# Optimization experiments

Measured on AMD Instinct MI355X. Metric: run time of the kernel, lower is better.

## Reference

```python
import jax, jax.numpy as jnp
import numpy as np

H = 8          # num_heads
T = 2          # num_edge_types
NEG_SLOPE = 0.2


def _edge_softmax(scores, dst, num_nodes):
    # softmax over incoming edges of each destination node, per head
    m = jax.ops.segment_max(scores, dst, num_segments=num_nodes)  # [N,H]
    e = jnp.exp(scores - m[dst])                                   # [E,H]
    s = jax.ops.segment_sum(e, dst, num_segments=num_nodes)        # [N,H]
    return e / s[dst]


def setup_inputs() -> dict:
    key = jax.random.key(0)
    ks = jax.random.split(key, 8)
    N, D, E = 50000, 128, 800000
    return {
        "x": jax.random.normal(ks[0], (N, D), dtype=jnp.float32),
        "w_u": jax.random.normal(ks[1], (H * T, D), dtype=jnp.float32) * (1.0 / np.sqrt(D)),
        "b_u": jax.random.normal(ks[2], (H * T,), dtype=jnp.float32) * 0.01,
        "w_v": jax.random.normal(ks[3], (H * T, D), dtype=jnp.float32) * (1.0 / np.sqrt(D)),
        "src_e0": jax.random.randint(ks[4], (E,), 0, N, dtype=jnp.int32),
        "dst_e0": jax.random.randint(ks[5], (E,), 0, N, dtype=jnp.int32),
        "src_e1": jax.random.randint(ks[6], (E,), 0, N, dtype=jnp.int32),
        "dst_e1": jax.random.randint(ks[7], (E,), 0, N, dtype=jnp.int32),
    }


def reference(x, w_u, b_u, w_v, src_e0, dst_e0, src_e1, dst_e1):
    N, D = x.shape
    head_dim = D // H
    scores_u = x @ w_u.T + b_u   # [N, H*T]
    scores_v = x @ w_v.T         # [N, H*T]
    xh = x.reshape(N, head_dim, H)  # matches torch reshape(-1, head_dim, num_heads)
    outs = [x]  # sep=True
    for t, (src, dst) in enumerate([(src_e0, dst_e0), (src_e1, dst_e1)]):
        u = scores_u[:, t * H:(t + 1) * H]
        v = scores_v[:, t * H:(t + 1) * H]
        s = u[src] + v[dst]                         # u_add_v -> [E,H]
        s = jnp.where(s >= 0, s, NEG_SLOPE * s)     # LeakyReLU(0.2)
        p = _edge_softmax(s, dst, N)                # [E,H]
        msg = xh[src] * p[:, None, :]               # u_mul_e -> [E,head_dim,H]
        agg = jax.ops.segment_sum(msg, dst, num_segments=N)  # [N,head_dim,H]
        outs.append(agg.reshape(N, D))
    return jnp.concatenate(outs, axis=-1)  # [N, D*(1+T)]
```

## Files before the change

kernel.cpp:

```cpp
#include <hip/hip_runtime.h>

#define NEG_SLOPE 0.2f
#define RSHIFT 5
#define RW     32
#define MAXNR  1600
#define CHUNKP 8192

__device__ __forceinline__ ushort f2bf(float f) {
    union { float f; unsigned u; } c; c.f = f;
    unsigned u = c.u;
    return (ushort)((u + 0x7fffu + ((u >> 16) & 1u)) >> 16);
}
__device__ __forceinline__ float bflo(unsigned u) { return __uint_as_float(u << 16); }
__device__ __forceinline__ float bfhi(unsigned u) { return __uint_as_float(u & 0xffff0000u); }

__global__ __launch_bounds__(256) void mega_kernel(
    const float* __restrict__ x, const float* __restrict__ wu,
    const float* __restrict__ bu, const float* __restrict__ wv,
    const int* __restrict__ s0, const int* __restrict__ d0,
    const int* __restrict__ s1, const int* __restrict__ d1,
    float* __restrict__ out, ushort* __restrict__ xbf,
    float* __restrict__ su, float* __restrict__ sv,
    int* __restrict__ gcur, unsigned* __restrict__ pairs,
    int N, int E, int nr, int cap, int scoreBlocks, int ppset)
{
    __shared__ __align__(16) float smemf[32 * 129 + 16 * 132];
    int* smi = (int*)smemf;
    float* wlds = smemf;
    float* xtile = smemf + 32 * 129;
    int tid = threadIdx.x;
    int bid = blockIdx.x;

    if (bid < 2 * ppset) {
        int pb = bid;
        int t = pb / ppset, c = pb % ppset;
        const int* ss = t ? s1 : s0;
        const int* dd = t ? d1 : d0;
        int beg = c * CHUNKP, end = min(E, beg + CHUNKP);
        int* lcnt = smi; int* gb = smi + MAXNR; int* lrun = smi + 2 * MAXNR;
        for (int i = tid; i < nr; i += 256) lcnt[i] = 0;
        __syncthreads();
        for (int e = beg + tid; e < end; e += 256)
            atomicAdd(&lcnt[dd[e] >> RSHIFT], 1);
        __syncthreads();
        for (int i = tid; i < nr; i += 256) {
            gb[i] = atomicAdd(&gcur[t * nr + i], lcnt[i]);
            lrun[i] = 0;
        }
        __syncthreads();
        unsigned* pt = pairs + (size_t)t * nr * cap;
        for (int e = beg + tid; e < end; e += 256) {
            int dst = dd[e], src = ss[e];
            int rr = dst >> RSHIFT;
            int pos = atomicAdd(&lrun[rr], 1);
            pt[(size_t)rr * cap + gb[rr] + pos] = ((unsigned)dst << 16) | (unsigned)src;
        }
        return;
    }
    int nb = bid - 2 * ppset;
    int base = nb * 16;
    for (int i = tid; i < 4096; i += 256) {
        int o = i >> 7, k = i & 127;
        wlds[o * 129 + k] = (o < 16) ? wu[i] : wv[i - 2048];
    }
    for (int i2 = tid; i2 < 512; i2 += 256) {
        int I = nb * 512 + i2;
        int nl = i2 >> 5, q = i2 & 31;
        int n = base + nl;
        float4 v = make_float4(0.f, 0.f, 0.f, 0.f);
        if (n < N) {
            v = ((const float4*)x)[I];
            ((float4*)out)[(size_t)n * 96 + q] = v;
            ushort4 b;
            b.x = f2bf(v.x); b.y = f2bf(v.y); b.z = f2bf(v.z); b.w = f2bf(v.w);
            *(ushort4*)(xbf + (size_t)I * 4) = b;
        }
        ((float4*)(xtile + nl * 132))[q] = v;
    }
    __syncthreads();
    int o = tid & 15;
    int nl = tid >> 4;
    int n = base + nl;
    if (n >= N) return;
    const float4* xr4 = (const float4*)(xtile + nl * 132);
    const float* wur = wlds + o * 129;
    const float* wvr = wlds + (16 + o) * 129;
    float au = 0.f, av = 0.f;
#pragma unroll
    for (int kk = 0; kk < 32; ++kk) {
        float4 xv = xr4[kk];
        int k = kk * 4;
        au = fmaf(xv.x, wur[k],     au);  av = fmaf(xv.x, wvr[k],     av);
        au = fmaf(xv.y, wur[k + 1], au);  av = fmaf(xv.y, wvr[k + 1], av);
        au = fmaf(xv.z, wur[k + 2], au);  av = fmaf(xv.z, wvr[k + 2], av);
        au = fmaf(xv.w, wur[k + 3], au);  av = fmaf(xv.w, wvr[k + 3], av);
    }
    su[n * 16 + o] = au + bu[o];
    sv[n * 16 + o] = av;
}

__global__ __launch_bounds__(256, 8) void buildagg_kernel(
    const ushort* __restrict__ xbf, const float* __restrict__ su,
    const float* __restrict__ sv, const int* __restrict__ gcur,
    const unsigned* __restrict__ pairs, float* __restrict__ out,
    int N, int E, int nr, int cap)
{
    __shared__ ushort srcs[768];
    __shared__ int offl[33];
    __shared__ int cursor[32];
    __shared__ __align__(16) float ev4[4][512];
    int r = blockIdx.x, t = blockIdx.y, tid = threadIdx.x;
    int m = gcur[t * nr + r];
    if (m > cap) m = cap;
    const unsigned* p = pairs + ((size_t)t * nr + r) * cap;

    if (tid < 32) cursor[tid] = 0;
    __syncthreads();
    for (int i = tid; i < m; i += 256)
        atomicAdd(&cursor[(p[i] >> 16) & (RW - 1)], 1);
    __syncthreads();
    if (tid < 32) {
        int v = cursor[tid];
        int incl = v;
#pragma unroll
        for (int d = 1; d < 32; d <<= 1) {
            int o = __shfl(incl, tid - d);
            if (tid >= d) incl += o;
        }
        offl[tid + 1] = incl;
        if (tid == 0) offl[0] = 0;
        cursor[tid] = incl - v;
    }
    __syncthreads();
    for (int i = tid; i < m; i += 256) {
        unsigned v = p[i];
        int pos = atomicAdd(&cursor[(v >> 16) & (RW - 1)], 1);
        srcs[pos] = (ushort)(v & 0xffffu);
    }
    __syncthreads();

    int wid = tid >> 6, lane = tid & 63;
    int h = lane & 7, e8 = lane >> 3;
    int g2 = lane >> 4, q16 = lane & 15;
    int j0 = q16 * 8;
    float* ev = ev4[wid];
    for (int ln = wid; ln < RW; ln += 4) {
        int n = (r << RSHIFT) + ln;
        if (n >= N) break;
        int beg = offl[ln], end = offl[ln + 1];
        float vh = sv[n * 16 + t * 8 + h];
        float a0 = 0.f, a1 = 0.f, a2 = 0.f, a3 = 0.f;
        float a4 = 0.f, a5 = 0.f, a6 = 0.f, a7 = 0.f;
        float l = 0.f;
        for (int cbeg = beg; cbeg < end; cbeg += 64) {
            int cnt = min(end - cbeg, 64);
            int gmax = (cnt + 7) >> 3;
            for (int g = 0; g < gmax; g += 2) {
                int ea = g * 8 + e8, eb = ea + 8;
                int sa = srcs[cbeg + ((ea < cnt) ? ea : 0)];
                int sb = srcs[cbeg + ((eb < cnt) ? eb : 0)];
                float fa = su[sa * 16 + t * 8 + h];
                float fb = su[sb * 16 + t * 8 + h];
                float sca = fa + vh;
                float scb = fb + vh;
                sca = (sca >= 0.f) ? sca : NEG_SLOPE * sca;
                scb = (scb >= 0.f) ? scb : NEG_SLOPE * scb;
                float eea = (ea < cnt) ? __expf(sca) : 0.f;
                float eeb = (eb < cnt) ? __expf(scb) : 0.f;
                l += eea;
                l += eeb;
                ev[ea * 8 + h] = eea;
                ev[eb * 8 + h] = eeb;
            }
            int quads = (cnt + 3) >> 2;
            for (int i4 = 0; i4 < quads; i4 += 2) {
                int e0 = (i4 << 2) + g2, e1 = e0 + 4;
                int sA = srcs[cbeg + ((e0 < cnt) ? e0 : 0)];
                int sB = srcs[cbeg + ((e1 < cnt) ? e1 : 0)];
                uint4 uA = *(const uint4*)(xbf + (size_t)sA * 128 + j0);
                uint4 uB = *(const uint4*)(xbf + (size_t)sB * 128 + j0);
                float4 pA0 = *(const float4*)(ev + e0 * 8);
                float4 pA1 = *(const float4*)(ev + e0 * 8 + 4);
                float4 pB0 = *(const float4*)(ev + e1 * 8);
                float4 pB1 = *(const float4*)(ev + e1 * 8 + 4);
                a0 = fmaf(bflo(uA.x), pA0.x, a0);
                a1 = fmaf(bfhi(uA.x), pA0.y, a1);
                a2 = fmaf(bflo(uA.y), pA0.z, a2);
                a3 = fmaf(bfhi(uA.y), pA0.w, a3);
                a4 = fmaf(bflo(uA.z), pA1.x, a4);
                a5 = fmaf(bfhi(uA.z), pA1.y, a5);
                a6 = fmaf(bflo(uA.w), pA1.z, a6);
                a7 = fmaf(bfhi(uA.w), pA1.w, a7);
                a0 = fmaf(bflo(uB.x), pB0.x, a0);
                a1 = fmaf(bfhi(uB.x), pB0.y, a1);
                a2 = fmaf(bflo(uB.y), pB0.z, a2);
                a3 = fmaf(bfhi(uB.y), pB0.w, a3);
                a4 = fmaf(bflo(uB.z), pB1.x, a4);
                a5 = fmaf(bfhi(uB.z), pB1.y, a5);
                a6 = fmaf(bflo(uB.w), pB1.z, a6);
                a7 = fmaf(bfhi(uB.w), pB1.w, a7);
            }
        }
        l += __shfl_xor(l, 8);
        l += __shfl_xor(l, 16);
        l += __shfl_xor(l, 32);
        float invl = (l > 0.f) ? (1.f / l) : 0.f;
        a0 += __shfl_xor(a0, 16); a0 += __shfl_xor(a0, 32);
        a1 += __shfl_xor(a1, 16); a1 += __shfl_xor(a1, 32);
        a2 += __shfl_xor(a2, 16); a2 += __shfl_xor(a2, 32);
        a3 += __shfl_xor(a3, 16); a3 += __shfl_xor(a3, 32);
        a4 += __shfl_xor(a4, 16); a4 += __shfl_xor(a4, 32);
        a5 += __shfl_xor(a5, 16); a5 += __shfl_xor(a5, 32);
        a6 += __shfl_xor(a6, 16); a6 += __shfl_xor(a6, 32);
        a7 += __shfl_xor(a7, 16); a7 += __shfl_xor(a7, 32);
        float ih0 = __shfl(invl, 0);
        float ih1 = __shfl(invl, 1);
        float ih2 = __shfl(invl, 2);
        float ih3 = __shfl(invl, 3);
        float ih4 = __shfl(invl, 4);
        float ih5 = __shfl(invl, 5);
        float ih6 = __shfl(invl, 6);
        float ih7 = __shfl(invl, 7);
        if (g2 == 0) {
            float* op = out + (size_t)n * 384 + 128 + (size_t)t * 128 + j0;
            *(float4*)op       = make_float4(a0 * ih0, a1 * ih1, a2 * ih2, a3 * ih3);
            *(float4*)(op + 4) = make_float4(a4 * ih4, a5 * ih5, a6 * ih6, a7 * ih7);
        }
    }
}

extern "C" void kernel_launch(void* const* d_in, const int* in_sizes, int n_in,
                              void* d_out, int out_size, void* d_ws, size_t ws_size,
                              hipStream_t stream)
{
    const float* x  = (const float*)d_in[0];
    const float* wu = (const float*)d_in[1];
    const float* bu = (const float*)d_in[2];
    const float* wv = (const float*)d_in[3];
    const int* s0 = (const int*)d_in[4];
    const int* d0 = (const int*)d_in[5];
    const int* s1 = (const int*)d_in[6];
    const int* d1 = (const int*)d_in[7];
    float* out = (float*)d_out;
    int N = in_sizes[0] / 128;
    int E = in_sizes[4];

    int nr = ((N - 1) >> RSHIFT) + 1;
    long long mean = (long long)RW * E / N;
    int cap = (int)(mean + mean / 4 + 64);

    char* ws = (char*)d_ws;
    size_t o = 0;
    auto alloc = [&](size_t bytes) -> void* {
        void* p = ws + o;
        o = (o + bytes + 255) & ~(size_t)255;
        return p;
    };
    float* su       = (float*)alloc((size_t)N * 16 * 4);
    float* sv       = (float*)alloc((size_t)N * 16 * 4);
    int* gcur       = (int*)alloc((size_t)2 * nr * 4);
    unsigned* pairs = (unsigned*)alloc((size_t)2 * nr * cap * 4);
    ushort* xbf     = (ushort*)alloc((size_t)N * 128 * 2);

    int scoreBlocks = (N + 15) / 16;
    int ppset       = (E + CHUNKP - 1) / CHUNKP;

    hipMemsetAsync(gcur, 0, (size_t)2 * nr * 4, stream);
    mega_kernel<<<scoreBlocks + 2 * ppset, 256, 0, stream>>>(
        x, wu, bu, wv, s0, d0, s1, d1, out, xbf, su, sv,
        gcur, pairs, N, E, nr, cap, scoreBlocks, ppset);
    buildagg_kernel<<<dim3(nr, 2), 256, 0, stream>>>(
        xbf, su, sv, gcur, pairs, out, N, E, nr, cap);
}
```

Before: 231.6 us.

## Assign each 16-lane group its own destination node in buildagg

Aggregation now gives each 16-lane quarter-wave its own destination node (two nodes per group) instead of one wavefront per node. Each lane vector-loads four heads of source scores, and the reductions across lanes become shorter. The packed pairs are also staged into shared memory once, so the global buffer is not read twice during bucketing. This is meant to cut idle lanes on low-degree nodes and remove the wide cross-lane reductions. In exchange it adds serial per-group loops over 16-edge chunks and a shared-memory exchange of the inverse softmax sums that has no explicit barrier.

```diff
diff --git a/kernel.cpp b/kernel.cpp
--- a/kernel.cpp
+++ b/kernel.cpp
@@ -108,16 +108,20 @@
     __shared__ ushort srcs[768];
     __shared__ int offl[33];
     __shared__ int cursor[32];
-    __shared__ __align__(16) float ev4[4][512];
+    __shared__ __align__(16) float evs[16 * 136];
+    __shared__ __align__(16) float linv[16 * 8];
     int r = blockIdx.x, t = blockIdx.y, tid = threadIdx.x;
     int m = gcur[t * nr + r];
     if (m > cap) m = cap;
     const unsigned* p = pairs + ((size_t)t * nr + r) * cap;
 
+    unsigned* pl = (unsigned*)evs;
+    for (int i = tid; i < m; i += 256)
+        pl[i] = p[i];
     if (tid < 32) cursor[tid] = 0;
     __syncthreads();
     for (int i = tid; i < m; i += 256)
-        atomicAdd(&cursor[(p[i] >> 16) & (RW - 1)], 1);
+        atomicAdd(&cursor[(pl[i] >> 16) & (RW - 1)], 1);
     __syncthreads();
     if (tid < 32) {
         int v = cursor[tid];
@@ -133,56 +137,62 @@
     }
     __syncthreads();
     for (int i = tid; i < m; i += 256) {
-        unsigned v = p[i];
+        unsigned v = pl[i];
         int pos = atomicAdd(&cursor[(v >> 16) & (RW - 1)], 1);
         srcs[pos] = (ushort)(v & 0xffffu);
     }
     __syncthreads();
 
     int wid = tid >> 6, lane = tid & 63;
-    int h = lane & 7, e8 = lane >> 3;
-    int g2 = lane >> 4, q16 = lane & 15;
-    int j0 = q16 * 8;
-    float* ev = ev4[wid];
-    for (int ln = wid; ln < RW; ln += 4) {
+    int g2 = lane >> 4, ql = lane & 15;
+    int gidx = (wid << 2) + g2;
+    int e_sub = ql >> 1;
+    int hh = (ql & 1) * 4;
+    float* evg = evs + gidx * 136;
+    float* lig = linv + gidx * 8;
+#pragma unroll
+    for (int which = 0; which < 2; ++which) {
+        int ln = gidx * 2 + which;
         int n = (r << RSHIFT) + ln;
-        if (n >= N) break;
-        int beg = offl[ln], end = offl[ln + 1];
-        float vh = sv[n * 16 + t * 8 + h];
+        bool act = (n < N);
+        int beg = act ? offl[ln] : 0;
+        int end = act ? offl[ln + 1] : 0;
+        float4 vh4 = make_float4(0.f, 0.f, 0.f, 0.f);
+        if (act) vh4 = *(const float4*)(sv + (size_t)n * 16 + t * 8 + hh);
         float a0 = 0.f, a1 = 0.f, a2 = 0.f, a3 = 0.f;
         float a4 = 0.f, a5 = 0.f, a6 = 0.f, a7 = 0.f;
-        float l = 0.f;
-        for (int cbeg = beg; cbeg < end; cbeg += 64) {
-            int cnt = min(end - cbeg, 64);
-            int gmax = (cnt + 7) >> 3;
-            for (int g = 0; g < gmax; g += 2) {
-                int ea = g * 8 + e8, eb = ea + 8;
-                int sa = srcs[cbeg + ((ea < cnt) ? ea : 0)];
-                int sb = srcs[cbeg + ((eb < cnt) ? eb : 0)];
-                float fa = su[sa * 16 + t * 8 + h];
-                float fb = su[sb * 16 + t * 8 + h];
-                float sca = fa + vh;
-                float scb = fb + vh;
-                sca = (sca >= 0.f) ? sca : NEG_SLOPE * sca;
-                scb = (scb >= 0.f) ? scb : NEG_SLOPE * scb;
-                float eea = (ea < cnt) ? __expf(sca) : 0.f;
-                float eeb = (eb < cnt) ? __expf(scb) : 0.f;
-                l += eea;
-                l += eeb;
-                ev[ea * 8 + h] = eea;
-                ev[eb * 8 + h] = eeb;
+        float4 l4 = make_float4(0.f, 0.f, 0.f, 0.f);
+        for (int cbeg = beg; cbeg < end; cbeg += 16) {
+            int cnt = min(end - cbeg, 16);
+#pragma unroll
+            for (int it = 0; it < 2; ++it) {
+                int e = it * 8 + e_sub;
+                bool valid = e < cnt;
+                int sidx = srcs[cbeg + (valid ? e : 0)];
+                float4 fu = *(const float4*)(su + (size_t)sidx * 16 + t * 8 + hh);
+                float sx = fu.x + vh4.x; sx = (sx >= 0.f) ? sx : NEG_SLOPE * sx;
+                float sy = fu.y + vh4.y; sy = (sy >= 0.f) ? sy : NEG_SLOPE * sy;
+                float sz = fu.z + vh4.z; sz = (sz >= 0.f) ? sz : NEG_SLOPE * sz;
+                float sw = fu.w + vh4.w; sw = (sw >= 0.f) ? sw : NEG_SLOPE * sw;
+                float4 ee;
+                ee.x = valid ? __expf(sx) : 0.f;
+                ee.y = valid ? __expf(sy) : 0.f;
+                ee.z = valid ? __expf(sz) : 0.f;
+                ee.w = valid ? __expf(sw) : 0.f;
+                l4.x += ee.x; l4.y += ee.y; l4.z += ee.z; l4.w += ee.w;
+                *(float4*)(evg + e * 8 + hh) = ee;
             }
-            int quads = (cnt + 3) >> 2;
-            for (int i4 = 0; i4 < quads; i4 += 2) {
-                int e0 = (i4 << 2) + g2, e1 = e0 + 4;
-                int sA = srcs[cbeg + ((e0 < cnt) ? e0 : 0)];
+            int nit = (cnt + 1) >> 1;
+            for (int it = 0; it < nit; ++it) {
+                int e0 = it * 2, e1 = e0 + 1;
+                int sA = srcs[cbeg + e0];
                 int sB = srcs[cbeg + ((e1 < cnt) ? e1 : 0)];
-                uint4 uA = *(const uint4*)(xbf + (size_t)sA * 128 + j0);
-                uint4 uB = *(const uint4*)(xbf + (size_t)sB * 128 + j0);
-                float4 pA0 = *(const float4*)(ev + e0 * 8);
-                float4 pA1 = *(const float4*)(ev + e0 * 8 + 4);
-                float4 pB0 = *(const float4*)(ev + e1 * 8);
-                float4 pB1 = *(const float4*)(ev + e1 * 8 + 4);
+                uint4 uA = *(const uint4*)(xbf + (size_t)sA * 128 + ql * 8);
+                uint4 uB = *(const uint4*)(xbf + (size_t)sB * 128 + ql * 8);
+                float4 pA0 = *(const float4*)(evg + e0 * 8);
+                float4 pA1 = *(const float4*)(evg + e0 * 8 + 4);
+                float4 pB0 = *(const float4*)(evg + e1 * 8);
+                float4 pB1 = *(const float4*)(evg + e1 * 8 + 4);
                 a0 = fmaf(bflo(uA.x), pA0.x, a0);
                 a1 = fmaf(bfhi(uA.x), pA0.y, a1);
                 a2 = fmaf(bflo(uA.y), pA0.z, a2);
@@ -201,30 +211,24 @@
                 a7 = fmaf(bfhi(uB.w), pB1.w, a7);
             }
         }
-        l += __shfl_xor(l, 8);
-        l += __shfl_xor(l, 16);
-        l += __shfl_xor(l, 32);
-        float invl = (l > 0.f) ? (1.f / l) : 0.f;
-        a0 += __shfl_xor(a0, 16); a0 += __shfl_xor(a0, 32);
-        a1 += __shfl_xor(a1, 16); a1 += __shfl_xor(a1, 32);
-        a2 += __shfl_xor(a2, 16); a2 += __shfl_xor(a2, 32);
-        a3 += __shfl_xor(a3, 16); a3 += __shfl_xor(a3, 32);
-        a4 += __shfl_xor(a4, 16); a4 += __shfl_xor(a4, 32);
-        a5 += __shfl_xor(a5, 16); a5 += __shfl_xor(a5, 32);
-        a6 += __shfl_xor(a6, 16); a6 += __shfl_xor(a6, 32);
-        a7 += __shfl_xor(a7, 16); a7 += __shfl_xor(a7, 32);
-        float ih0 = __shfl(invl, 0);
-        float ih1 = __shfl(invl, 1);
-        float ih2 = __shfl(invl, 2);
-        float ih3 = __shfl(invl, 3);
-        float ih4 = __shfl(invl, 4);
-        float ih5 = __shfl(invl, 5);
-        float ih6 = __shfl(invl, 6);
-        float ih7 = __shfl(invl, 7);
-        if (g2 == 0) {
-            float* op = out + (size_t)n * 384 + 128 + (size_t)t * 128 + j0;
-            *(float4*)op       = make_float4(a0 * ih0, a1 * ih1, a2 * ih2, a3 * ih3);
-            *(float4*)(op + 4) = make_float4(a4 * ih4, a5 * ih5, a6 * ih6, a7 * ih7);
+        l4.x += __shfl_xor(l4.x, 2);  l4.y += __shfl_xor(l4.y, 2);
+        l4.z += __shfl_xor(l4.z, 2);  l4.w += __shfl_xor(l4.w, 2);
+        l4.x += __shfl_xor(l4.x, 4);  l4.y += __shfl_xor(l4.y, 4);
+        l4.z += __shfl_xor(l4.z, 4);  l4.w += __shfl_xor(l4.w, 4);
+        l4.x += __shfl_xor(l4.x, 8);  l4.y += __shfl_xor(l4.y, 8);
+        l4.z += __shfl_xor(l4.z, 8);  l4.w += __shfl_xor(l4.w, 8);
+        float4 inv;
+        inv.x = (l4.x > 0.f) ? (1.f / l4.x) : 0.f;
+        inv.y = (l4.y > 0.f) ? (1.f / l4.y) : 0.f;
+        inv.z = (l4.z > 0.f) ? (1.f / l4.z) : 0.f;
+        inv.w = (l4.w > 0.f) ? (1.f / l4.w) : 0.f;
+        if (ql < 2) *(float4*)(lig + hh) = inv;
+        float4 il0 = *(const float4*)(lig);
+        float4 il1 = *(const float4*)(lig + 4);
+        if (act) {
+            float* op = out + (size_t)n * 384 + 128 + (size_t)t * 128 + ql * 8;
+            *(float4*)op       = make_float4(a0 * il0.x, a1 * il0.y, a2 * il0.z, a3 * il0.w);
+            *(float4*)(op + 4) = make_float4(a4 * il1.x, a5 * il1.y, a6 * il1.z, a7 * il1.w);
         }
     }
 }
```

New measurement: 282.4 us. +21.9%, slower.

## Vectorize score gathers and weight loads, halve partition chunk size

Applied to the files above, without the earlier changes.

The edge-score phase now has each lane handle 4 heads of one edge with float4 loads of su and sv, instead of one scalar per lane, which cuts gather instructions and widens the softmax-sum reduction. The score GEMV now loads weights as float4 with a 132 stride and uses split accumulators for more ILP. The partition chunk size is halved to launch more partition blocks. The head-sum reduction grows to more shuffle steps, and the LDS stride of 132 may bring bank conflicts.

```diff
diff --git a/kernel.cpp b/kernel.cpp
--- a/kernel.cpp
+++ b/kernel.cpp
@@ -4,7 +4,7 @@
 #define RSHIFT 5
 #define RW     32
 #define MAXNR  1600
-#define CHUNKP 8192
+#define CHUNKP 4096
 
 __device__ __forceinline__ ushort f2bf(float f) {
     union { float f; unsigned u; } c; c.f = f;
@@ -24,10 +24,10 @@
     int* __restrict__ gcur, unsigned* __restrict__ pairs,
     int N, int E, int nr, int cap, int scoreBlocks, int ppset)
 {
-    __shared__ __align__(16) float smemf[32 * 129 + 16 * 132];
+    __shared__ __align__(16) float smemf[32 * 132 + 16 * 132];
     int* smi = (int*)smemf;
     float* wlds = smemf;
-    float* xtile = smemf + 32 * 129;
+    float* xtile = smemf + 32 * 132;
     int tid = threadIdx.x;
     int bid = blockIdx.x;
 
@@ -59,9 +59,10 @@
     }
     int nb = bid - 2 * ppset;
     int base = nb * 16;
-    for (int i = tid; i < 4096; i += 256) {
-        int o = i >> 7, k = i & 127;
-        wlds[o * 129 + k] = (o < 16) ? wu[i] : wv[i - 2048];
+    for (int i = tid; i < 1024; i += 256) {
+        int o = i >> 5, k4 = i & 31;
+        float4 w = (o < 16) ? ((const float4*)wu)[i] : ((const float4*)wv)[i - 512];
+        *(float4*)(wlds + o * 132 + k4 * 4) = w;
     }
     for (int i2 = tid; i2 < 512; i2 += 256) {
         int I = nb * 512 + i2;
@@ -83,20 +84,22 @@
     int n = base + nl;
     if (n >= N) return;
     const float4* xr4 = (const float4*)(xtile + nl * 132);
-    const float* wur = wlds + o * 129;
-    const float* wvr = wlds + (16 + o) * 129;
-    float au = 0.f, av = 0.f;
+    const float4* wur4 = (const float4*)(wlds + o * 132);
+    const float4* wvr4 = (const float4*)(wlds + (16 + o) * 132);
+    float au0 = 0.f, au1 = 0.f, au2 = 0.f, au3 = 0.f;
+    float av0 = 0.f, av1 = 0.f, av2 = 0.f, av3 = 0.f;
 #pragma unroll
     for (int kk = 0; kk < 32; ++kk) {
         float4 xv = xr4[kk];
-        int k = kk * 4;
-        au = fmaf(xv.x, wur[k],     au);  av = fmaf(xv.x, wvr[k],     av);
-        au = fmaf(xv.y, wur[k + 1], au);  av = fmaf(xv.y, wvr[k + 1], av);
-        au = fmaf(xv.z, wur[k + 2], au);  av = fmaf(xv.z, wvr[k + 2], av);
-        au = fmaf(xv.w, wur[k + 3], au);  av = fmaf(xv.w, wvr[k + 3], av);
-    }
-    su[n * 16 + o] = au + bu[o];
-    sv[n * 16 + o] = av;
+        float4 wuv = wur4[kk];
+        float4 wvv = wvr4[kk];
+        au0 = fmaf(xv.x, wuv.x, au0);  av0 = fmaf(xv.x, wvv.x, av0);
+        au1 = fmaf(xv.y, wuv.y, au1);  av1 = fmaf(xv.y, wvv.y, av1);
+        au2 = fmaf(xv.z, wuv.z, au2);  av2 = fmaf(xv.z, wvv.z, av2);
+        au3 = fmaf(xv.w, wuv.w, au3);  av3 = fmaf(xv.w, wvv.w, av3);
+    }
+    su[n * 16 + o] = ((au0 + au1) + (au2 + au3)) + bu[o];
+    sv[n * 16 + o] = (av0 + av1) + (av2 + av3);
 }
 
 __global__ __launch_bounds__(256, 8) void buildagg_kernel(
@@ -140,37 +143,38 @@
     __syncthreads();
 
     int wid = tid >> 6, lane = tid & 63;
-    int h = lane & 7, e8 = lane >> 3;
     int g2 = lane >> 4, q16 = lane & 15;
     int j0 = q16 * 8;
+    int eg = lane >> 1;
+    int hh = (lane & 1) * 4;
     float* ev = ev4[wid];
     for (int ln = wid; ln < RW; ln += 4) {
         int n = (r << RSHIFT) + ln;
         if (n >= N) break;
         int beg = offl[ln], end = offl[ln + 1];
-        float vh = sv[n * 16 + t * 8 + h];
+        float4 vh4 = *(const float4*)(sv + (size_t)n * 16 + t * 8 + hh);
         float a0 = 0.f, a1 = 0.f, a2 = 0.f, a3 = 0.f;
         float a4 = 0.f, a5 = 0.f, a6 = 0.f, a7 = 0.f;
-        float l = 0.f;
+        float4 l4 = make_float4(0.f, 0.f, 0.f, 0.f);
         for (int cbeg = beg; cbeg < end; cbeg += 64) {
             int cnt = min(end - cbeg, 64);
-            int gmax = (cnt + 7) >> 3;
-            for (int g = 0; g < gmax; g += 2) {
-                int ea = g * 8 + e8, eb = ea + 8;
-                int sa = srcs[cbeg + ((ea < cnt) ? ea : 0)];
-                int sb = srcs[cbeg + ((eb < cnt) ? eb : 0)];
-                float fa = su[sa * 16 + t * 8 + h];
-                float fb = su[sb * 16 + t * 8 + h];
-                float sca = fa + vh;
-                float scb = fb + vh;
-                sca = (sca >= 0.f) ? sca : NEG_SLOPE * sca;
-                scb = (scb >= 0.f) ? scb : NEG_SLOPE * scb;
-                float eea = (ea < cnt) ? __expf(sca) : 0.f;
-                float eeb = (eb < cnt) ? __expf(scb) : 0.f;
-                l += eea;
-                l += eeb;
-                ev[ea * 8 + h] = eea;
-                ev[eb * 8 + h] = eeb;
+            int gmax = (cnt + 31) >> 5;
+            for (int g = 0; g < gmax; ++g) {
+                int e = g * 32 + eg;
+                bool valid = e < cnt;
+                int sidx = srcs[cbeg + (valid ? e : 0)];
+                float4 fu = *(const float4*)(su + (size_t)sidx * 16 + t * 8 + hh);
+                float sx = fu.x + vh4.x; sx = (sx >= 0.f) ? sx : NEG_SLOPE * sx;
+                float sy = fu.y + vh4.y; sy = (sy >= 0.f) ? sy : NEG_SLOPE * sy;
+                float sz = fu.z + vh4.z; sz = (sz >= 0.f) ? sz : NEG_SLOPE * sz;
+                float sw = fu.w + vh4.w; sw = (sw >= 0.f) ? sw : NEG_SLOPE * sw;
+                float4 ee;
+                ee.x = valid ? __expf(sx) : 0.f;
+                ee.y = valid ? __expf(sy) : 0.f;
+                ee.z = valid ? __expf(sz) : 0.f;
+                ee.w = valid ? __expf(sw) : 0.f;
+                l4.x += ee.x; l4.y += ee.y; l4.z += ee.z; l4.w += ee.w;
+                *(float4*)(ev + e * 8 + hh) = ee;
             }
             int quads = (cnt + 3) >> 2;
             for (int i4 = 0; i4 < quads; i4 += 2) {
@@ -201,10 +205,21 @@
                 a7 = fmaf(bfhi(uB.w), pB1.w, a7);
             }
         }
-        l += __shfl_xor(l, 8);
-        l += __shfl_xor(l, 16);
-        l += __shfl_xor(l, 32);
-        float invl = (l > 0.f) ? (1.f / l) : 0.f;
+        l4.x += __shfl_xor(l4.x, 2);  l4.y += __shfl_xor(l4.y, 2);
+        l4.z += __shfl_xor(l4.z, 2);  l4.w += __shfl_xor(l4.w, 2);
+        l4.x += __shfl_xor(l4.x, 4);  l4.y += __shfl_xor(l4.y, 4);
+        l4.z += __shfl_xor(l4.z, 4);  l4.w += __shfl_xor(l4.w, 4);
+        l4.x += __shfl_xor(l4.x, 8);  l4.y += __shfl_xor(l4.y, 8);
+        l4.z += __shfl_xor(l4.z, 8);  l4.w += __shfl_xor(l4.w, 8);
+        l4.x += __shfl_xor(l4.x, 16); l4.y += __shfl_xor(l4.y, 16);
+        l4.z += __shfl_xor(l4.z, 16); l4.w += __shfl_xor(l4.w, 16);
+        l4.x += __shfl_xor(l4.x, 32); l4.y += __shfl_xor(l4.y, 32);
+        l4.z += __shfl_xor(l4.z, 32); l4.w += __shfl_xor(l4.w, 32);
+        float4 invl4;
+        invl4.x = (l4.x > 0.f) ? (1.f / l4.x) : 0.f;
+        invl4.y = (l4.y > 0.f) ? (1.f / l4.y) : 0.f;
+        invl4.z = (l4.z > 0.f) ? (1.f / l4.z) : 0.f;
+        invl4.w = (l4.w > 0.f) ? (1.f / l4.w) : 0.f;
         a0 += __shfl_xor(a0, 16); a0 += __shfl_xor(a0, 32);
         a1 += __shfl_xor(a1, 16); a1 += __shfl_xor(a1, 32);
         a2 += __shfl_xor(a2, 16); a2 += __shfl_xor(a2, 32);
@@ -213,14 +228,14 @@
         a5 += __shfl_xor(a5, 16); a5 += __shfl_xor(a5, 32);
         a6 += __shfl_xor(a6, 16); a6 += __shfl_xor(a6, 32);
         a7 += __shfl_xor(a7, 16); a7 += __shfl_xor(a7, 32);
-        float ih0 = __shfl(invl, 0);
-        float ih1 = __shfl(invl, 1);
-        float ih2 = __shfl(invl, 2);
-        float ih3 = __shfl(invl, 3);
-        float ih4 = __shfl(invl, 4);
-        float ih5 = __shfl(invl, 5);
-        float ih6 = __shfl(invl, 6);
-        float ih7 = __shfl(invl, 7);
+        float ih0 = __shfl(invl4.x, 0);
+        float ih1 = __shfl(invl4.y, 0);
+        float ih2 = __shfl(invl4.z, 0);
+        float ih3 = __shfl(invl4.w, 0);
+        float ih4 = __shfl(invl4.x, 1);
+        float ih5 = __shfl(invl4.y, 1);
+        float ih6 = __shfl(invl4.z, 1);
+        float ih7 = __shfl(invl4.w, 1);
         if (g2 == 0) {
             float* op = out + (size_t)n * 384 + 128 + (size_t)t * 128 + j0;
             *(float4*)op       = make_float4(a0 * ih0, a1 * ih1, a2 * ih2, a3 * ih3);
```

Measured after the change: 250.1 us. +8.0%, slower.
